# Optimization experiments

Hardware: AMD Instinct MI355X
Metric: run time of the kernel (lower is better)

## Reference

```python
import jax, jax.numpy as jnp
import numpy as np

RES = (64, 64)
TEMP = 0.1  # forward default temp

def _mgrid(res):
    # matches torch.meshgrid(linspace(0, r-1, r)...) with default 'ij' indexing
    gs = jnp.meshgrid(*[jnp.arange(r, dtype=jnp.float32) for r in res], indexing='ij')
    return jnp.stack(gs, 0)  # [2, H, W]

def setup_inputs() -> dict:
    key = jax.random.key(0)
    k1, k2 = jax.random.split(key)
    x = jax.random.normal(k1, (8, 32, RES[0], RES[1]), dtype=jnp.float32)
    of = jax.random.normal(k2, (8, 2, RES[0], RES[1]), dtype=jnp.float32)
    return {"x": x, "of": of}

def reference(x, of):
    bs, C = x.shape[0], x.shape[1]
    hw = RES[0] * RES[1]
    gpos = _mgrid(RES).reshape(2, hw)                 # [2, HW] target pixel positions
    opos = gpos[None] + of.reshape(bs, 2, hw)         # [bs, 2, HW] flow-displaced source positions
    # L1 distance: logits[b, i, j] = sum_c |opos[b, c, j] - gpos[c, i]|
    dist = jnp.abs(opos[:, :, None, :] - gpos[None, :, :, None]).sum(axis=1)  # [bs, HW, HW]
    # softmax over target axis i (dim=-2 in torch) -> each source pixel j distributes mass over targets
    locs = jax.nn.softmax(-dist / TEMP, axis=1)       # [bs, HW, HW]
    # out[b, c, i] = sum_j x[b, c, j] * locs[b, i, j]
    out = jnp.einsum('bij,bcj->bci', locs, x.reshape(bs, C, hw))
    return out.reshape(bs, C, RES[0], RES[1])
```

## Files before the change

### kernel.cpp

```cpp
#include <hip/hip_runtime.h>
#include <hip/hip_fp16.h>
#include <math.h>

#define HW    4096
#define NC    32
#define NB    8
#define TINV  10.0f
#define RWIN  8
#define WDIM  (8 + 2 * RWIN)
#define NSRC  (WDIM * WDIM)
#define RCUT  2.0f


__device__ __forceinline__ __half2 u32_as_h2(unsigned int u) {
    union { unsigned int u; __half2 h; } c; c.u = u; return c.h;
}
__device__ __forceinline__ unsigned int h2_as_u32(__half2 h) {
    union { __half2 h; unsigned int u; } c; c.h = h; return c.u;
}

__global__ __launch_bounds__(256) void warp_fused_kernel(
    const float* __restrict__ x, const float* __restrict__ of,
    float* __restrict__ out)
{
    __shared__ float4       pw[NSRC];
    __shared__ unsigned int xw[NSRC * 8];
    __shared__ float4       wp[4][65];
    __shared__ int          sj[4][64];

    const int b    = blockIdx.z;
    const int h    = blockIdx.y;
    const int tile = blockIdx.x;
    const int ty0  = (tile >> 3) << 3;
    const int tx0  = (tile & 7) << 3;
    const int tid  = threadIdx.x;
    const int lane = tid & 63;
    const int wv   = __builtin_amdgcn_readfirstlane(tid >> 6);

    for (int s = tid; s < NSRC; s += 256) {
        int wr = s / WDIM, wc = s - wr * WDIM;
        int jy = ty0 - RWIN + wr, jx = tx0 - RWIN + wc;
        float4 pv = make_float4(0.f, 0.f, 0.f, 0.f);
        if (((unsigned)jy < 64u) && ((unsigned)jx < 64u)) {
            int j = (jy << 6) + jx;
            float oy = (float)jy + of[(b * 2 + 0) * HW + j];
            float ox = (float)jx + of[(b * 2 + 1) * HW + j];
            int cy0 = min(max((int)floorf(oy), 0), 63);
            int cx0 = min(max((int)floorf(ox), 0), 63);
            float Dy = 0.f, Dx = 0.f;
            #pragma unroll
            for (int d = -3; d <= 3; ++d) {
                int iy2 = cy0 + d, ix2 = cx0 + d;
                if ((unsigned)iy2 < 64u) Dy += __expf(-TINV * fabsf(oy - (float)iy2));
                if ((unsigned)ix2 < 64u) Dx += __expf(-TINV * fabsf(ox - (float)ix2));
            }
            pv = make_float4(oy, ox, 1.f / Dy, 1.f / Dx);
        }
        pw[s] = pv;
    }

    const float* xb = x + ((size_t)((b * NC) + (h << 4)) << 12);
    for (int i = tid; i < 8 * WDIM * 6; i += 256) {
        int pr  = i / (WDIM * 6);
        int rem = i - pr * (WDIM * 6);
        int row = rem / 6, seg = rem - row * 6;
        int jy  = ty0 - RWIN + row;
        int jx0 = tx0 - RWIN + (seg << 2);
        unsigned int q0 = 0, q1 = 0, q2 = 0, q3 = 0;
        if (((unsigned)jy < 64u) && ((unsigned)jx0 < 61u)) {
            const float* src = xb + ((2 * pr) << 12) + (jy << 6) + jx0;
            float4 a = *(const float4*)src;
            float4 c = *(const float4*)(src + HW);
            q0 = h2_as_u32(__floats2half2_rn(a.x, c.x));
            q1 = h2_as_u32(__floats2half2_rn(a.y, c.y));
            q2 = h2_as_u32(__floats2half2_rn(a.z, c.z));
            q3 = h2_as_u32(__floats2half2_rn(a.w, c.w));
        }
        unsigned int* d = &xw[((row * WDIM + (seg << 2)) << 3) + pr];
        d[0] = q0; d[8] = q1; d[16] = q2; d[24] = q3;
    }

    __syncthreads();

    const float iy = (float)(ty0 + (lane >> 3));
    const float ix = (float)(tx0 + (lane & 7));

    __half2 acc8[8];
    #pragma unroll
    for (int c = 0; c < 8; ++c) acc8[c] = __floats2half2_rn(0.f, 0.f);

    const int srow = lane >> 5;
    const int scol = lane & 31;

    for (int r = 0; r < 3; ++r) {
        int ry = wv + srow * 4 + r * 8;
        int jy = ty0 - RWIN + ry;
        int jx = tx0 - RWIN + scol;
        bool valid = ((unsigned)jy < 64u) && ((unsigned)jx < 64u) && (scol < WDIM);
        int ws = ry * WDIM + min(scol, WDIM - 1);
        float4 p = pw[ws];
        float cy = fminf(fmaxf(p.x, 0.f), 63.f);
        float cx = fminf(fmaxf(p.y, 0.f), 63.f);
        float dyr = fmaxf(fmaxf((float)ty0 - cy, cy - ((float)ty0 + 7.f)), 0.f);
        float dxr = fmaxf(fmaxf((float)tx0 - cx, cx - ((float)tx0 + 7.f)), 0.f);
        bool pred = valid && (dyr + dxr < RCUT);

        unsigned long long m = __ballot(pred);
        int cnt = __popcll(m);
        if (pred) {
            int pos = __builtin_amdgcn_mbcnt_hi((unsigned)(m >> 32),
                      __builtin_amdgcn_mbcnt_lo((unsigned)m, 0u));
            wp[wv][pos] = p;
            sj[wv][pos] = ws;
        }
        if (lane == cnt) { wp[wv][cnt] = make_float4(1.f, 1.f, 0.f, 0.f); sj[wv][cnt] = 0; }
        int cntp = cnt + (cnt & 1);

        for (int k = 0; k < cntp; k += 2) {
            float4 p0 = wp[wv][k], p1 = wp[wv][k + 1];
            const uint4* x0 = (const uint4*)&xw[sj[wv][k]     << 3];
            const uint4* x1 = (const uint4*)&xw[sj[wv][k + 1] << 3];
            uint4 A0 = x0[0], A1 = x0[1];
            uint4 B0 = x1[0], B1 = x1[1];

            float g0 = (__expf(-TINV * fabsf(p0.x - iy)) * p0.z)
                     * (__expf(-TINV * fabsf(p0.y - ix)) * p0.w);
            float g1 = (__expf(-TINV * fabsf(p1.x - iy)) * p1.z)
                     * (__expf(-TINV * fabsf(p1.y - ix)) * p1.w);
            __half2 hg0 = __float2half2_rn(g0);
            __half2 hg1 = __float2half2_rn(g1);

            acc8[0] = __hfma2(hg0, u32_as_h2(A0.x), acc8[0]);
            acc8[1] = __hfma2(hg0, u32_as_h2(A0.y), acc8[1]);
            acc8[2] = __hfma2(hg0, u32_as_h2(A0.z), acc8[2]);
            acc8[3] = __hfma2(hg0, u32_as_h2(A0.w), acc8[3]);
            acc8[4] = __hfma2(hg0, u32_as_h2(A1.x), acc8[4]);
            acc8[5] = __hfma2(hg0, u32_as_h2(A1.y), acc8[5]);
            acc8[6] = __hfma2(hg0, u32_as_h2(A1.z), acc8[6]);
            acc8[7] = __hfma2(hg0, u32_as_h2(A1.w), acc8[7]);

            acc8[0] = __hfma2(hg1, u32_as_h2(B0.x), acc8[0]);
            acc8[1] = __hfma2(hg1, u32_as_h2(B0.y), acc8[1]);
            acc8[2] = __hfma2(hg1, u32_as_h2(B0.z), acc8[2]);
            acc8[3] = __hfma2(hg1, u32_as_h2(B0.w), acc8[3]);
            acc8[4] = __hfma2(hg1, u32_as_h2(B1.x), acc8[4]);
            acc8[5] = __hfma2(hg1, u32_as_h2(B1.y), acc8[5]);
            acc8[6] = __hfma2(hg1, u32_as_h2(B1.z), acc8[6]);
            acc8[7] = __hfma2(hg1, u32_as_h2(B1.w), acc8[7]);
        }
    }

    __syncthreads();
    unsigned int* redu = (unsigned int*)pw;
    unsigned int* myr  = redu + ((wv << 6) + lane) * 9;
    #pragma unroll
    for (int c = 0; c < 8; ++c) myr[c] = h2_as_u32(acc8[c]);
    __syncthreads();

    int c2  = tid >> 5;
    int t32 = tid & 31;
    #pragma unroll
    for (int k = 0; k < 2; ++k) {
        int t = t32 + 32 * k;
        float sx = 0.f, sy = 0.f;
        #pragma unroll
        for (int w = 0; w < 4; ++w) {
            float2 f = __half22float2(u32_as_h2(redu[((w << 6) + t) * 9 + c2]));
            sx += f.x; sy += f.y;
        }
        int ch   = (h << 4) + 2 * c2;
        int base = (((b << 5) + ch) << 12) + (ty0 + (t >> 3)) * 64 + (tx0 + (t & 7));
        out[base]      = sx;
        out[base + HW] = sy;
    }
}

extern "C" void kernel_launch(void* const* d_in, const int* in_sizes, int n_in,
                              void* d_out, int out_size, void* d_ws, size_t ws_size,
                              hipStream_t stream) {
    const float* x  = (const float*)d_in[0];
    const float* of = (const float*)d_in[1];
    float* out = (float*)d_out;
    (void)d_ws; (void)ws_size;

    warp_fused_kernel<<<dim3(64, 2, NB), dim3(256), 0, stream>>>(x, of, out);
}
```

Before: 73.47 us.

## Split into prep kernel for params and fp16 channel-interleaved x, then gather

Adds a prep kernel that computes the per-source softmax normalizers once per pixel and transposes x into a pixel-major, channel-interleaved half2 layout in workspace. The gather kernel then loads precomputed params and contiguous 16-byte chunks per pixel instead of recomputing normalizers for every halo tile and converting strided fp32 loads. This removes redundant exp work on overlapping halos and makes the window loads vector-friendly. In exchange it adds a second launch and a global round trip through workspace.

```diff
diff --git a/kernel.cpp b/kernel.cpp
--- a/kernel.cpp
+++ b/kernel.cpp
@@ -19,8 +19,53 @@
     union { __half2 h; unsigned int u; } c; c.h = h; return c.u;
 }
 
-__global__ __launch_bounds__(256) void warp_fused_kernel(
+__global__ __launch_bounds__(256) void prep_kernel(
     const float* __restrict__ x, const float* __restrict__ of,
+    float4* __restrict__ params, __half2* __restrict__ xt2)
+{
+    __shared__ float tile[16][66];
+    const int bx   = blockIdx.x;
+    const int half = blockIdx.y;
+    const int b    = bx >> 6;
+    const int j0   = (bx & 63) << 6;
+    const int t    = threadIdx.x;
+    const int ch0  = half << 4;
+    const int jj   = t & 63;
+    const int c4   = t >> 6;
+
+    if (half == 0 && t < 64) {
+        int j = j0 + t;
+        float oy = (float)(j >> 6) + of[(b * 2 + 0) * HW + j];
+        float ox = (float)(j & 63) + of[(b * 2 + 1) * HW + j];
+        int cy0 = min(max((int)floorf(oy), 0), 63);
+        int cx0 = min(max((int)floorf(ox), 0), 63);
+        float Dy = 0.f, Dx = 0.f;
+        #pragma unroll
+        for (int d = -3; d <= 3; ++d) {
+            int iy = cy0 + d, ix = cx0 + d;
+            if ((unsigned)iy < 64u) Dy += __expf(-TINV * fabsf(oy - (float)iy));
+            if ((unsigned)ix < 64u) Dx += __expf(-TINV * fabsf(ox - (float)ix));
+        }
+        params[(b << 12) + j] = make_float4(oy, ox, 1.f / Dy, 1.f / Dx);
+    }
+
+    #pragma unroll
+    for (int k = 0; k < 4; ++k) {
+        int c = c4 * 4 + k;
+        tile[c][jj] = x[((size_t)(b * NC + ch0 + c) << 12) + j0 + jj];
+    }
+    __syncthreads();
+    #pragma unroll
+    for (int k = 0; k < 2; ++k) {
+        int s  = k * 256 + t;
+        int j2 = s >> 3, pr = s & 7;
+        xt2[((size_t)((b << 12) + j0 + j2) << 4) + (half << 3) + pr] =
+            __floats2half2_rn(tile[2 * pr][j2], tile[2 * pr + 1][j2]);
+    }
+}
+
+__global__ __launch_bounds__(256) void gather_kernel(
+    const float4* __restrict__ params, const unsigned int* __restrict__ xtu,
     float* __restrict__ out)
 {
     __shared__ float4       pw[NSRC];
@@ -37,47 +82,23 @@
     const int lane = tid & 63;
     const int wv   = __builtin_amdgcn_readfirstlane(tid >> 6);
 
+    const float4* pb = params + (b << 12);
     for (int s = tid; s < NSRC; s += 256) {
         int wr = s / WDIM, wc = s - wr * WDIM;
         int jy = ty0 - RWIN + wr, jx = tx0 - RWIN + wc;
-        float4 pv = make_float4(0.f, 0.f, 0.f, 0.f);
-        if (((unsigned)jy < 64u) && ((unsigned)jx < 64u)) {
-            int j = (jy << 6) + jx;
-            float oy = (float)jy + of[(b * 2 + 0) * HW + j];
-            float ox = (float)jx + of[(b * 2 + 1) * HW + j];
-            int cy0 = min(max((int)floorf(oy), 0), 63);
-            int cx0 = min(max((int)floorf(ox), 0), 63);
-            float Dy = 0.f, Dx = 0.f;
-            #pragma unroll
-            for (int d = -3; d <= 3; ++d) {
-                int iy2 = cy0 + d, ix2 = cx0 + d;
-                if ((unsigned)iy2 < 64u) Dy += __expf(-TINV * fabsf(oy - (float)iy2));
-                if ((unsigned)ix2 < 64u) Dx += __expf(-TINV * fabsf(ox - (float)ix2));
-            }
-            pv = make_float4(oy, ox, 1.f / Dy, 1.f / Dx);
-        }
-        pw[s] = pv;
-    }
-
-    const float* xb = x + ((size_t)((b * NC) + (h << 4)) << 12);
-    for (int i = tid; i < 8 * WDIM * 6; i += 256) {
-        int pr  = i / (WDIM * 6);
-        int rem = i - pr * (WDIM * 6);
-        int row = rem / 6, seg = rem - row * 6;
-        int jy  = ty0 - RWIN + row;
-        int jx0 = tx0 - RWIN + (seg << 2);
-        unsigned int q0 = 0, q1 = 0, q2 = 0, q3 = 0;
-        if (((unsigned)jy < 64u) && ((unsigned)jx0 < 61u)) {
-            const float* src = xb + ((2 * pr) << 12) + (jy << 6) + jx0;
-            float4 a = *(const float4*)src;
-            float4 c = *(const float4*)(src + HW);
-            q0 = h2_as_u32(__floats2half2_rn(a.x, c.x));
-            q1 = h2_as_u32(__floats2half2_rn(a.y, c.y));
-            q2 = h2_as_u32(__floats2half2_rn(a.z, c.z));
-            q3 = h2_as_u32(__floats2half2_rn(a.w, c.w));
-        }
-        unsigned int* d = &xw[((row * WDIM + (seg << 2)) << 3) + pr];
-        d[0] = q0; d[8] = q1; d[16] = q2; d[24] = q3;
+        bool v = ((unsigned)jy < 64u) && ((unsigned)jx < 64u);
+        pw[s] = v ? pb[(jy << 6) + jx] : make_float4(0.f, 0.f, 0.f, 0.f);
+    }
+
+    const unsigned int* xb = xtu + ((size_t)(b << 12) << 4) + (h << 3);
+    for (int i = tid; i < 2 * NSRC; i += 256) {
+        int src = i >> 1, e = i & 1;
+        int wr = src / WDIM, wc = src - wr * WDIM;
+        int jy = ty0 - RWIN + wr, jx = tx0 - RWIN + wc;
+        bool v = ((unsigned)jy < 64u) && ((unsigned)jx < 64u);
+        uint4 q = make_uint4(0u, 0u, 0u, 0u);
+        if (v) q = *(const uint4*)(xb + (((size_t)((jy << 6) + jx)) << 4) + (e << 2));
+        *(uint4*)&xw[(size_t)i << 2] = q;
     }
 
     __syncthreads();
@@ -118,8 +139,9 @@
 
         for (int k = 0; k < cntp; k += 2) {
             float4 p0 = wp[wv][k], p1 = wp[wv][k + 1];
-            const uint4* x0 = (const uint4*)&xw[sj[wv][k]     << 3];
-            const uint4* x1 = (const uint4*)&xw[sj[wv][k + 1] << 3];
+            int s0 = sj[wv][k], s1 = sj[wv][k + 1];
+            const uint4* x0 = (const uint4*)&xw[(size_t)s0 << 3];
+            const uint4* x1 = (const uint4*)&xw[(size_t)s1 << 3];
             uint4 A0 = x0[0], A1 = x0[1];
             uint4 B0 = x1[0], B1 = x1[1];
 
@@ -181,7 +203,11 @@
     const float* x  = (const float*)d_in[0];
     const float* of = (const float*)d_in[1];
     float* out = (float*)d_out;
-    (void)d_ws; (void)ws_size;
-
-    warp_fused_kernel<<<dim3(64, 2, NB), dim3(256), 0, stream>>>(x, of, out);
-}
+
+    float4*  params = (float4*)d_ws;
+    __half2* xt2    = (__half2*)((char*)d_ws + NB * HW * sizeof(float4));
+
+    prep_kernel<<<dim3(NB * 64, 2), dim3(256), 0, stream>>>(x, of, params, xt2);
+    gather_kernel<<<dim3(64, 2, NB), dim3(256), 0, stream>>>(
+        params, (const unsigned int*)xt2, out);
+}
```

Result: faster. 69.52 us (-5.4%).
